# Performance work log

Measured on AMD Instinct MI355X. Metric: run time of the kernel, lower is better.

Reference implementation:

```python
import math
import jax, jax.numpy as jnp
import numpy as np

N_HEAD = 16

def setup_inputs() -> dict:
    key = jax.random.key(0)
    k1, k2, k3 = jax.random.split(key, 3)
    B, T, C = 4, 2048, 1024
    x = jax.random.normal(k1, (B, T, C), dtype=jnp.float32)
    Wqkv = jax.random.normal(k2, (C, 3 * C), dtype=jnp.float32) * (1.0 / math.sqrt(C))
    bqkv = jnp.zeros((3 * C,), dtype=jnp.float32)
    Wproj = jax.random.normal(k3, (C, C), dtype=jnp.float32) * (1.0 / math.sqrt(C))
    bproj = jnp.zeros((C,), dtype=jnp.float32)
    return {"x": x, "Wqkv": Wqkv, "bqkv": bqkv, "Wproj": Wproj, "bproj": bproj}

def reference(x, Wqkv, bqkv, Wproj, bproj):
    B, T, C = x.shape
    H = N_HEAD
    D = C // H
    # fused QKV projection
    qkv = x @ Wqkv + bqkv                      # [B,T,3C]
    qkv = qkv.reshape(B, T, 3, H, D).transpose(0, 2, 3, 1, 4)  # [B,3,H,T,D]
    q, k, v = qkv[:, 0], qkv[:, 1], qkv[:, 2]  # each [B,H,T,D]
    scale = 1.0 / math.sqrt(D)
    att = jnp.einsum('bhtd,bhsd->bhts', q, k) * scale  # [B,H,T,T]
    # causal mask: disallow s > t
    mask = jnp.triu(jnp.ones((T, T), dtype=bool), k=1)
    att = jnp.where(mask, jnp.float32(-1e9), att)
    att = jax.nn.softmax(att, axis=-1)
    y = jnp.einsum('bhts,bhsd->bhtd', att, v)  # [B,H,T,D]
    y = y.transpose(0, 2, 1, 3).reshape(B, T, C)
    y = y @ Wproj + bproj
    return y
```

## Files before the change

### kernel.cpp

```cpp
#include <hip/hip_runtime.h>
#include <hip/hip_bf16.h>

#define B_ 4
#define T_ 2048
#define C_ 1024
#define H_ 16
#define D_ 64

typedef __attribute__((ext_vector_type(8))) short short8;
typedef __attribute__((ext_vector_type(4))) float f32x4;

#define QSCALE 0.18033688011112042f

static __device__ __forceinline__ unsigned short f2bf(float f) {
  unsigned u = __float_as_uint(f);
  u += 0x7fff + ((u >> 16) & 1);
  return (unsigned short)(u >> 16);
}

static __device__ __forceinline__ unsigned cvt_pk_bf16(float lo, float hi) {
  unsigned r;
  asm("v_cvt_pk_bf16_f32 %0, %1, %2" : "=v"(r) : "v"(lo), "v"(hi));
  return r;
}

static __device__ __forceinline__ float fast_exp2(float x) {
#if __has_builtin(__builtin_amdgcn_exp2f)
  return __builtin_amdgcn_exp2f(x);
#else
  return exp2f(x);
#endif
}

#define GL2LDS16(g, l)                                              \
  __builtin_amdgcn_global_load_lds(                                 \
      (const __attribute__((address_space(1))) void*)(g),           \
      (__attribute__((address_space(3))) void*)(l), 16, 0, 0)

__global__ __launch_bounds__(256) void prepass(
    const float* __restrict__ x, const float* __restrict__ Wq,
    const float* __restrict__ Wp, ushort* __restrict__ xb,
    ushort* __restrict__ Wqt, ushort* __restrict__ Wpt) {
  __shared__ ushort tile[32][33];
  const int bid = blockIdx.x;
  if (bid < 8192) {
    const size_t i = ((size_t)bid * 256 + threadIdx.x) * 4;
    float4 vv = *(const float4*)(x + i);
    ushort4 o = {f2bf(vv.x), f2bf(vv.y), f2bf(vv.z), f2bf(vv.w)};
    *(ushort4*)(xb + i) = o;
    return;
  }
  const float* in;
  ushort* out;
  int N, tix;
  if (bid < 8192 + 3072) {
    in = Wq; out = Wqt; N = 3 * C_; tix = bid - 8192;
  } else {
    in = Wp; out = Wpt; N = C_; tix = bid - 11264;
  }
  const int nT = N >> 5;
  const int k0 = (tix / nT) << 5, n0 = (tix % nT) << 5;
  const int r = threadIdx.x >> 3;
  const int c4 = (threadIdx.x & 7) << 2;
  float4 v = *(const float4*)(in + (size_t)(k0 + r) * N + n0 + c4);
  tile[c4 + 0][r] = f2bf(v.x);
  tile[c4 + 1][r] = f2bf(v.y);
  tile[c4 + 2][r] = f2bf(v.z);
  tile[c4 + 3][r] = f2bf(v.w);
  __syncthreads();
  ushort4 o = {tile[r][c4], tile[r][c4 + 1], tile[r][c4 + 2], tile[r][c4 + 3]};
  *(ushort4*)(out + (size_t)(n0 + r) * C_ + k0 + c4) = o;
}

static __device__ __forceinline__ void swz_src64(int wave, int lane, int p,
                                                 int& row, int& offU) {
  const int flat = p * 4096 + wave * 1024 + lane * 16;
  row = flat >> 7;
  const int pos = (flat & 127) >> 4;
  const int x = pos ^ (row & 7);
  offU = x * 8;
}
static __device__ __forceinline__ int swz_frag64(int r, int quad, int ko) {
  return r * 128 + (((quad | (ko << 2)) ^ (r & 7)) << 4);
}

__global__ __launch_bounds__(256) void gemm_qkv_mfma(
    const ushort* __restrict__ A, const ushort* __restrict__ Bt,
    const float* __restrict__ bias, ushort* __restrict__ q,
    ushort* __restrict__ k, ushort* __restrict__ v) {
  __shared__ __align__(16) ushort As[128 * 64];
  __shared__ __align__(16) ushort Bs[128 * 64];
  const int tid = threadIdx.x;
  const int wave = tid >> 6, lane = tid & 63;
  const int c = lane & 15, quad = lane >> 4;
  const int wm = wave & 1, wn = wave >> 1;
  const int bid0 = blockIdx.y * 24 + blockIdx.x;
  const int bid = (bid0 & 7) * 192 + (bid0 >> 3);
  const int m0 = (bid / 24) << 7;
  const int n0 = (bid % 24) << 7;

  int sRow[4], sOff[4];
#pragma unroll
  for (int p = 0; p < 4; ++p) swz_src64(wave, lane, p, sRow[p], sOff[p]);
  int fOffA[2][4], fOffB[2][4];
#pragma unroll
  for (int ko = 0; ko < 2; ++ko) {
#pragma unroll
    for (int i = 0; i < 4; ++i)
      fOffA[ko][i] = swz_frag64(wm * 64 + i * 16 + c, quad, ko);
#pragma unroll
    for (int j = 0; j < 4; ++j)
      fOffB[ko][j] = swz_frag64(wn * 64 + j * 16 + c, quad, ko);
  }

  f32x4 acc[4][4];
#pragma unroll
  for (int i = 0; i < 4; ++i)
#pragma unroll
    for (int j = 0; j < 4; ++j) acc[i][j] = (f32x4){0.f, 0.f, 0.f, 0.f};

  for (int k0 = 0; k0 < C_; k0 += 64) {
    __syncthreads();
#pragma unroll
    for (int p = 0; p < 4; ++p) {
      GL2LDS16(A + (size_t)(m0 + sRow[p]) * C_ + k0 + sOff[p],
               (char*)As + p * 4096 + wave * 1024);
      GL2LDS16(Bt + (size_t)(n0 + sRow[p]) * C_ + k0 + sOff[p],
               (char*)Bs + p * 4096 + wave * 1024);
    }
    __syncthreads();
#pragma unroll
    for (int ko = 0; ko < 2; ++ko) {
      short8 af[4], bf[4];
#pragma unroll
      for (int i = 0; i < 4; ++i)
        af[i] = *(const short8*)((const char*)As + fOffA[ko][i]);
#pragma unroll
      for (int j = 0; j < 4; ++j)
        bf[j] = *(const short8*)((const char*)Bs + fOffB[ko][j]);
#pragma unroll
      for (int i = 0; i < 4; ++i)
#pragma unroll
        for (int j = 0; j < 4; ++j)
          acc[i][j] = __builtin_amdgcn_mfma_f32_16x16x32_bf16(af[i], bf[j],
                                                              acc[i][j], 0, 0, 0);
    }
  }

  const int s = n0 >> 10;
  if (s == 2) {
#pragma unroll
    for (int j = 0; j < 4; ++j) {
      const int n = n0 + wn * 64 + j * 16 + c;
      const int h = (n >> 6) & 15, d = n & 63;
      const float bval = bias[n];
#pragma unroll
      for (int i = 0; i < 4; ++i) {
        const int m = m0 + wm * 64 + i * 16 + quad * 4;
        const int b = m >> 11, t = m & 2047;
        ushort4 pk = {f2bf(acc[i][j][0] + bval), f2bf(acc[i][j][1] + bval),
                      f2bf(acc[i][j][2] + bval), f2bf(acc[i][j][3] + bval)};
        *(ushort4*)(v + (((size_t)((b << 4) + h) << 6) + d) * T_ + t) = pk;
      }
    }
  } else {
    ushort* outp = (s == 0) ? q : k;
    const float sc = (s == 0) ? QSCALE : 1.0f;
#pragma unroll
    for (int j = 0; j < 4; ++j) {
      const int n = n0 + wn * 64 + j * 16 + c;
      const int h = (n >> 6) & 15, d = n & 63;
      const float bval = bias[n];
#pragma unroll
      for (int i = 0; i < 4; ++i) {
#pragma unroll
        for (int r = 0; r < 4; ++r) {
          const int m = m0 + wm * 64 + i * 16 + quad * 4 + r;
          const int b = m >> 11, t = m & 2047;
          outp[(((size_t)((b << 4) + h) << 11) + t) * 64 + d] =
              f2bf((acc[i][j][r] + bval) * sc);
        }
      }
    }
  }
}

__global__ __launch_bounds__(256) void gemm_proj_mfma(
    const ushort* __restrict__ A, const ushort* __restrict__ Bt,
    const float* __restrict__ bias, float* __restrict__ out) {
  __shared__ __align__(16) ushort As[128 * 64];
  __shared__ __align__(16) ushort Bs[128 * 64];
  const int tid = threadIdx.x;
  const int wave = tid >> 6, lane = tid & 63;
  const int c = lane & 15, quad = lane >> 4;
  const int wm = wave & 1, wn = wave >> 1;
  const int bid0 = blockIdx.y * 8 + blockIdx.x;
  const int bid = (bid0 & 7) * 64 + (bid0 >> 3);
  const int m0 = (bid >> 3) << 7;
  const int n0 = (bid & 7) << 7;

  int sRow[4], sOff[4];
#pragma unroll
  for (int p = 0; p < 4; ++p) swz_src64(wave, lane, p, sRow[p], sOff[p]);
  int fOffA[2][4], fOffB[2][4];
#pragma unroll
  for (int ko = 0; ko < 2; ++ko) {
#pragma unroll
    for (int i = 0; i < 4; ++i)
      fOffA[ko][i] = swz_frag64(wm * 64 + i * 16 + c, quad, ko);
#pragma unroll
    for (int j = 0; j < 4; ++j)
      fOffB[ko][j] = swz_frag64(wn * 64 + j * 16 + c, quad, ko);
  }

  f32x4 acc[4][4];
#pragma unroll
  for (int i = 0; i < 4; ++i)
#pragma unroll
    for (int j = 0; j < 4; ++j) acc[i][j] = (f32x4){0.f, 0.f, 0.f, 0.f};

  for (int k0 = 0; k0 < C_; k0 += 64) {
    __syncthreads();
#pragma unroll
    for (int p = 0; p < 4; ++p) {
      GL2LDS16(A + (size_t)(m0 + sRow[p]) * C_ + k0 + sOff[p],
               (char*)As + p * 4096 + wave * 1024);
      GL2LDS16(Bt + (size_t)(n0 + sRow[p]) * C_ + k0 + sOff[p],
               (char*)Bs + p * 4096 + wave * 1024);
    }
    __syncthreads();
#pragma unroll
    for (int ko = 0; ko < 2; ++ko) {
      short8 af[4], bf[4];
#pragma unroll
      for (int i = 0; i < 4; ++i)
        af[i] = *(const short8*)((const char*)As + fOffA[ko][i]);
#pragma unroll
      for (int j = 0; j < 4; ++j)
        bf[j] = *(const short8*)((const char*)Bs + fOffB[ko][j]);
#pragma unroll
      for (int i = 0; i < 4; ++i)
#pragma unroll
        for (int j = 0; j < 4; ++j)
          acc[i][j] = __builtin_amdgcn_mfma_f32_16x16x32_bf16(af[i], bf[j],
                                                              acc[i][j], 0, 0, 0);
    }
  }

#pragma unroll
  for (int j = 0; j < 4; ++j) {
    const int n = n0 + wn * 64 + j * 16 + c;
    const float bval = bias[n];
#pragma unroll
    for (int i = 0; i < 4; ++i) {
#pragma unroll
      for (int r = 0; r < 4; ++r) {
        const int m = m0 + wm * 64 + i * 16 + quad * 4 + r;
        out[(size_t)m * C_ + n] = acc[i][j][r] + bval;
      }
    }
  }
}

__global__ __launch_bounds__(256) void attn(const ushort* __restrict__ q,
                                            const ushort* __restrict__ k,
                                            const ushort* __restrict__ v,
                                            ushort* __restrict__ y2) {
  static const int qt_tab[16] = {15, 14, 13, 12, 8, 9, 10, 11,
                                 4,  5,  6,  7,  3, 2, 1,  0};
  const int qt = qt_tab[blockIdx.x >> 6];
  const int bh = blockIdx.x & 63;
  const int t0 = qt << 7;
  const int w = threadIdx.x >> 6;
  const int lane = threadIdx.x & 63;
  const int c = lane & 15;
  const int quad = lane >> 4;

  const ushort* qp = q + (size_t)bh * T_ * D_;
  const ushort* kp = k + (size_t)bh * T_ * D_;
  const ushort* vp = v + (size_t)bh * D_ * T_;

  __shared__ __align__(16) ushort Ks[64][72];
  __shared__ __align__(16) ushort Vs[64][72];
  __shared__ __align__(16) ushort Ps[4][32][72];

  short8 qf[2][2];
#pragma unroll
  for (int g = 0; g < 2; ++g) {
    const ushort* qrow = qp + (size_t)(t0 + 32 * w + 16 * g + c) * D_;
    qf[g][0] = *(const short8*)(qrow + quad * 8);
    qf[g][1] = *(const short8*)(qrow + 32 + quad * 8);
  }

  const int srow = threadIdx.x >> 2;
  const int soff = (threadIdx.x & 3) << 4;

  uint4 ka, kb, va, vb;
  {
    const ushort* ks = kp + (size_t)srow * D_ + soff;
    const ushort* vs = vp + (size_t)srow * T_ + soff;
    ka = *(const uint4*)(ks);
    kb = *(const uint4*)(ks + 8);
    va = *(const uint4*)(vs);
    vb = *(const uint4*)(vs + 8);
  }

  f32x4 o[2][4];
  float l_i[2] = {0.f, 0.f};
#pragma unroll
  for (int g = 0; g < 2; ++g)
#pragma unroll
    for (int dt = 0; dt < 4; ++dt) o[g][dt] = (f32x4){0.f, 0.f, 0.f, 0.f};

  const int nb = 2 * qt + 2;
  for (int ib = 0; ib < nb; ++ib) {
    const int s0 = ib << 6;
    __syncthreads();
    *(uint4*)(&Ks[srow][soff]) = ka;
    *(uint4*)(&Ks[srow][soff + 8]) = kb;
    *(uint4*)(&Vs[srow][soff]) = va;
    *(uint4*)(&Vs[srow][soff + 8]) = vb;
    __syncthreads();

    if (ib + 1 < nb) {
      const int s1 = (ib + 1) << 6;
      const ushort* ks = kp + (size_t)(s1 + srow) * D_ + soff;
      const ushort* vs = vp + (size_t)srow * T_ + s1 + soff;
      ka = *(const uint4*)(ks);
      kb = *(const uint4*)(ks + 8);
      va = *(const uint4*)(vs);
      vb = *(const uint4*)(vs + 8);
    }

    f32x4 st[2][4];
    __builtin_amdgcn_s_setprio(1);
#pragma unroll
    for (int kt = 0; kt < 4; ++kt) {
      short8 af0 = *(const short8*)(&Ks[kt * 16 + c][quad * 8]);
      short8 af1 = *(const short8*)(&Ks[kt * 16 + c][32 + quad * 8]);
#pragma unroll
      for (int g = 0; g < 2; ++g) {
        f32x4 a = (f32x4){0.f, 0.f, 0.f, 0.f};
        a = __builtin_amdgcn_mfma_f32_16x16x32_bf16(af0, qf[g][0], a, 0, 0, 0);
        a = __builtin_amdgcn_mfma_f32_16x16x32_bf16(af1, qf[g][1], a, 0, 0, 0);
        st[g][kt] = a;
      }
    }
    __builtin_amdgcn_s_setprio(0);

#pragma unroll
    for (int g = 0; g < 2; ++g) {
      const int qbase = t0 + 32 * w + 16 * g;
      if (s0 + 63 > qbase) {
#pragma unroll
        for (int kt = 0; kt < 4; ++kt)
#pragma unroll
          for (int r = 0; r < 4; ++r)
            if (s0 + kt * 16 + 4 * quad + r > qbase + c) st[g][kt][r] = -1e30f;
      }
      float lacc = 0.f;
#pragma unroll
      for (int kt = 0; kt < 4; ++kt) {
        float p0 = fast_exp2(st[g][kt][0]);
        float p1 = fast_exp2(st[g][kt][1]);
        float p2 = fast_exp2(st[g][kt][2]);
        float p3 = fast_exp2(st[g][kt][3]);
        lacc += (p0 + p1) + (p2 + p3);
        uint2 pw = {cvt_pk_bf16(p0, p1), cvt_pk_bf16(p2, p3)};
        *(uint2*)(&Ps[w][g * 16 + c][kt * 16 + 4 * quad]) = pw;
      }
      l_i[g] += lacc;
    }

    short8 pf[2][2];
#pragma unroll
    for (int g = 0; g < 2; ++g) {
      pf[g][0] = *(const short8*)(&Ps[w][g * 16 + c][quad * 8]);
      pf[g][1] = *(const short8*)(&Ps[w][g * 16 + c][32 + quad * 8]);
    }
    __builtin_amdgcn_s_setprio(1);
#pragma unroll
    for (int dt = 0; dt < 4; ++dt) {
      short8 vf0 = *(const short8*)(&Vs[dt * 16 + c][quad * 8]);
      short8 vf1 = *(const short8*)(&Vs[dt * 16 + c][32 + quad * 8]);
#pragma unroll
      for (int g = 0; g < 2; ++g) {
        o[g][dt] =
            __builtin_amdgcn_mfma_f32_16x16x32_bf16(vf0, pf[g][0], o[g][dt], 0, 0, 0);
        o[g][dt] =
            __builtin_amdgcn_mfma_f32_16x16x32_bf16(vf1, pf[g][1], o[g][dt], 0, 0, 0);
      }
    }
    __builtin_amdgcn_s_setprio(0);
  }

  float linv[2];
#pragma unroll
  for (int g = 0; g < 2; ++g) {
    float ls = l_i[g];
    ls += __shfl_xor(ls, 16);
    ls += __shfl_xor(ls, 32);
    linv[g] = 1.0f / ls;
  }

  const int b = bh >> 4, h = bh & 15;
#pragma unroll
  for (int g = 0; g < 2; ++g) {
    const int row = t0 + 32 * w + 16 * g + c;
    ushort* dst = y2 + (size_t)(b * T_ + row) * C_ + h * 64;
#pragma unroll
    for (int dt = 0; dt < 4; ++dt) {
      uint2 ov = {cvt_pk_bf16(o[g][dt][0] * linv[g], o[g][dt][1] * linv[g]),
                  cvt_pk_bf16(o[g][dt][2] * linv[g], o[g][dt][3] * linv[g])};
      *(uint2*)(dst + dt * 16 + 4 * quad) = ov;
    }
  }
}

extern "C" void kernel_launch(void* const* d_in, const int* in_sizes, int n_in,
                              void* d_out, int out_size, void* d_ws,
                              size_t ws_size, hipStream_t stream) {
  const float* x = (const float*)d_in[0];
  const float* Wqkv = (const float*)d_in[1];
  const float* bqkv = (const float*)d_in[2];
  const float* Wproj = (const float*)d_in[3];
  const float* bproj = (const float*)d_in[4];
  float* out = (float*)d_out;

  const size_t per = (size_t)B_ * H_ * T_ * D_;
  ushort* q = (ushort*)d_ws;
  ushort* k = q + per;
  ushort* v = k + per;
  ushort* y2 = v + per;
  ushort* xb = y2 + per;
  ushort* Wqkvt = xb + per;
  ushort* Wprojt = Wqkvt + 3 * C_ * C_;

  prepass<<<dim3(12288), 256, 0, stream>>>(x, Wqkv, Wproj, xb, Wqkvt, Wprojt);
  gemm_qkv_mfma<<<dim3(24, 64), 256, 0, stream>>>(xb, Wqkvt, bqkv, q, k, v);
  attn<<<dim3(1024), 256, 0, stream>>>(q, k, v, y2);
  gemm_proj_mfma<<<dim3(8, 64), 256, 0, stream>>>(y2, Wprojt, bproj, out);
}
```

Before: 261.4 us.

## Double-buffer attention K/V tiles via direct global-to-LDS loads with swizzle

The attention kernel now stages K and V tiles straight from global memory into two swizzled LDS buffers, using a direct global-to-LDS load macro, instead of loading into registers and then writing LDS. This removes one barrier per iteration and the register round trip, and overlaps the next tile's load with compute. It also replaces the padded layout with an XOR swizzle to avoid bank conflicts, and simplifies the q-tile ordering to a plain descending order, which may change load balance across blocks. The kernel relies on the helpers GL2LDS16 and swz_frag64 being defined in the part of the file not shown. With a single barrier per iteration, correctness depends on the async LDS loads being waited on before that barrier.

```diff
diff --git a/kernel.cpp b/kernel.cpp
--- a/kernel.cpp
+++ b/kernel.cpp
@@ -266,9 +266,7 @@
                                             const ushort* __restrict__ k,
                                             const ushort* __restrict__ v,
                                             ushort* __restrict__ y2) {
-  static const int qt_tab[16] = {15, 14, 13, 12, 8, 9, 10, 11,
-                                 4,  5,  6,  7,  3, 2, 1,  0};
-  const int qt = qt_tab[blockIdx.x >> 6];
+  const int qt = 15 - (int)(blockIdx.x >> 6);
   const int bh = blockIdx.x & 63;
   const int t0 = qt << 7;
   const int w = threadIdx.x >> 6;
@@ -280,8 +278,8 @@
   const ushort* kp = k + (size_t)bh * T_ * D_;
   const ushort* vp = v + (size_t)bh * D_ * T_;
 
-  __shared__ __align__(16) ushort Ks[64][72];
-  __shared__ __align__(16) ushort Vs[64][72];
+  __shared__ __align__(16) ushort Ks[2][64 * 64];
+  __shared__ __align__(16) ushort Vs[2][64 * 64];
   __shared__ __align__(16) ushort Ps[4][32][72];
 
   short8 qf[2][2];
@@ -292,18 +290,23 @@
     qf[g][1] = *(const short8*)(qrow + 32 + quad * 8);
   }
 
-  const int srow = threadIdx.x >> 2;
-  const int soff = (threadIdx.x & 3) << 4;
-
-  uint4 ka, kb, va, vb;
-  {
-    const ushort* ks = kp + (size_t)srow * D_ + soff;
-    const ushort* vs = vp + (size_t)srow * T_ + soff;
-    ka = *(const uint4*)(ks);
-    kb = *(const uint4*)(ks + 8);
-    va = *(const uint4*)(vs);
-    vb = *(const uint4*)(vs + 8);
-  }
+  int sRow[2], sX[2];
+#pragma unroll
+  for (int p = 0; p < 2; ++p) {
+    const int flat = p * 4096 + (int)threadIdx.x * 16;
+    sRow[p] = flat >> 7;
+    sX[p] = (((flat & 127) >> 4) ^ (sRow[p] & 7)) * 8;
+  }
+
+#define STAGE(buf, s0s)                                                   \
+  do {                                                                    \
+    _Pragma("unroll") for (int p = 0; p < 2; ++p) {                       \
+      GL2LDS16(kp + (size_t)((s0s) + sRow[p]) * D_ + sX[p],               \
+               (char*)Ks[buf] + p * 4096 + w * 1024);                     \
+      GL2LDS16(vp + (size_t)sRow[p] * T_ + (s0s) + sX[p],                 \
+               (char*)Vs[buf] + p * 4096 + w * 1024);                     \
+    }                                                                     \
+  } while (0)
 
   f32x4 o[2][4];
   float l_i[2] = {0.f, 0.f};
@@ -313,31 +316,21 @@
     for (int dt = 0; dt < 4; ++dt) o[g][dt] = (f32x4){0.f, 0.f, 0.f, 0.f};
 
   const int nb = 2 * qt + 2;
+  STAGE(0, 0);
+  int cur = 0;
+
   for (int ib = 0; ib < nb; ++ib) {
     const int s0 = ib << 6;
     __syncthreads();
-    *(uint4*)(&Ks[srow][soff]) = ka;
-    *(uint4*)(&Ks[srow][soff + 8]) = kb;
-    *(uint4*)(&Vs[srow][soff]) = va;
-    *(uint4*)(&Vs[srow][soff + 8]) = vb;
-    __syncthreads();
-
-    if (ib + 1 < nb) {
-      const int s1 = (ib + 1) << 6;
-      const ushort* ks = kp + (size_t)(s1 + srow) * D_ + soff;
-      const ushort* vs = vp + (size_t)srow * T_ + s1 + soff;
-      ka = *(const uint4*)(ks);
-      kb = *(const uint4*)(ks + 8);
-      va = *(const uint4*)(vs);
-      vb = *(const uint4*)(vs + 8);
-    }
+    if (ib + 1 < nb) STAGE(cur ^ 1, s0 + 64);
 
     f32x4 st[2][4];
     __builtin_amdgcn_s_setprio(1);
 #pragma unroll
     for (int kt = 0; kt < 4; ++kt) {
-      short8 af0 = *(const short8*)(&Ks[kt * 16 + c][quad * 8]);
-      short8 af1 = *(const short8*)(&Ks[kt * 16 + c][32 + quad * 8]);
+      const char* kb = (const char*)Ks[cur];
+      short8 af0 = *(const short8*)(kb + swz_frag64(kt * 16 + c, quad, 0));
+      short8 af1 = *(const short8*)(kb + swz_frag64(kt * 16 + c, quad, 1));
 #pragma unroll
       for (int g = 0; g < 2; ++g) {
         f32x4 a = (f32x4){0.f, 0.f, 0.f, 0.f};
@@ -381,8 +374,9 @@
     __builtin_amdgcn_s_setprio(1);
 #pragma unroll
     for (int dt = 0; dt < 4; ++dt) {
-      short8 vf0 = *(const short8*)(&Vs[dt * 16 + c][quad * 8]);
-      short8 vf1 = *(const short8*)(&Vs[dt * 16 + c][32 + quad * 8]);
+      const char* vb = (const char*)Vs[cur];
+      short8 vf0 = *(const short8*)(vb + swz_frag64(dt * 16 + c, quad, 0));
+      short8 vf1 = *(const short8*)(vb + swz_frag64(dt * 16 + c, quad, 1));
 #pragma unroll
       for (int g = 0; g < 2; ++g) {
         o[g][dt] =
@@ -392,7 +386,9 @@
       }
     }
     __builtin_amdgcn_s_setprio(0);
-  }
+    cur ^= 1;
+  }
+#undef STAGE
 
   float linv[2];
 #pragma unroll
```

New measurement: 244.2 us. -6.6%, faster.
